# Optimization experiments

Hardware: AMD Instinct MI355X
Metric: run time of the kernel (lower is better)

## Reference

```python
import jax, jax.numpy as jnp
import numpy as np

DIM = 1024
H = 56
NS = 32            # n_state == head_v_dim
KEY_DIM = H * NS   # 1792
D_INNER = H * NS   # 1792
T_LEN = 2048
B = 4


def _xavier(key, fan_out, fan_in):
    bound = (6.0 / (fan_in + fan_out)) ** 0.5
    return jax.random.uniform(key, (fan_out, fan_in), jnp.float32, -bound, bound)


def setup_inputs() -> dict:
    key = jax.random.key(0)
    ks = jax.random.split(key, 8)
    x = jax.random.normal(ks[0], (T_LEN, B, DIM), jnp.float32)
    S = jnp.zeros((B, H, NS, NS), jnp.float32)
    Wq = _xavier(ks[1], KEY_DIM, DIM)
    Wk = _xavier(ks[2], KEY_DIM, DIM)
    Wv = _xavier(ks[3], D_INNER, DIM)
    Wa = _xavier(ks[4], H, DIM)
    Wout = _xavier(ks[5], DIM, D_INNER)
    A_log = jax.random.uniform(ks[6], (H,), jnp.float32, -5.0, -1.0)
    dt_bias = jax.random.uniform(ks[7], (H,), jnp.float32, 0.5, 1.5)
    return {"x": x, "S": S, "Wq": Wq, "Wk": Wk, "Wv": Wv, "Wa": Wa,
            "A_log": A_log, "dt_bias": dt_bias, "Wout": Wout}


def _l2norm(t):
    # matches F.normalize(dim=-1): x / max(||x||, 1e-12)
    n = jnp.sqrt(jnp.sum(t * t, axis=-1, keepdims=True))
    return t / jnp.maximum(n, 1e-12)


def reference(x, S, Wq, Wk, Wv, Wa, A_log, dt_bias, Wout):
    T, Bb, _ = x.shape
    q = jax.nn.silu(x @ Wq.T).reshape(T, Bb, H, NS)
    k = jax.nn.silu(x @ Wk.T).reshape(T, Bb, H, NS)
    v = jax.nn.silu(x @ Wv.T).reshape(T, Bb, H, NS)
    q = _l2norm(q)
    k = _l2norm(k)
    a = x @ Wa.T                                   # [T,B,H]
    dt = jax.nn.softplus(a + dt_bias)
    decay = jnp.exp(-jnp.exp(A_log) * dt)          # [T,B,H]

    def step(S_t, inp):
        k_t, v_t, q_t, d_t = inp                   # [B,H,NS], [B,H,NS], [B,H,NS], [B,H]
        retrieved = jnp.einsum('bhij,bhi->bhj', S_t, k_t)   # S^T k
        delta = v_t - retrieved
        outer = k_t[..., :, None] * delta[..., None, :]     # [B,H,NS,NS] = k ox delta
        S_t = S_t + jnp.tanh(d_t[..., None, None] * S_t + outer)
        Sq = jnp.einsum('bhij,bhi->bhj', S_t, q_t)
        return S_t, Sq

    S_new, out = jax.lax.scan(step, S, (k, v, q, decay))
    out = out.reshape(T, Bb, D_INNER) @ Wout.T     # [T,B,dim]
    return out, S_new
```

## Files before the change

kernel.cpp:

```cpp
#include <hip/hip_runtime.h>


typedef __attribute__((ext_vector_type(8))) __bf16 bf16x8;
typedef __attribute__((ext_vector_type(8))) _Float16 f16x8;
typedef __attribute__((ext_vector_type(4))) float f32x4;
typedef __attribute__((ext_vector_type(2))) float f32x2;

#define T_LEN 2048
#define BB 4
#define HH 56
#define NS 32
#define DIM 1024
#define KD 1792
#define MROWS 8192
#define CH 16
#define NCHUNK (T_LEN / CH)

#define VMCNT(N) asm volatile("s_waitcnt vmcnt(" #N ")" ::: "memory")
#define LGKM(N)  asm volatile("s_waitcnt lgkmcnt(" #N ")" ::: "memory")
#define SB       __builtin_amdgcn_sched_barrier(0)

__device__ __forceinline__ float bf2f(unsigned short u) {
    return __uint_as_float(((unsigned int)u) << 16);
}
__device__ __forceinline__ unsigned short f2bf(float f) {
    unsigned int u = __float_as_uint(f);
    u += 0x7fffu + ((u >> 16) & 1u);
    return (unsigned short)(u >> 16);
}
__device__ __forceinline__ unsigned short f2h(float f) {
    union { _Float16 h; unsigned short u; } cv;
    cv.h = (_Float16)f;
    return cv.u;
}
__device__ __forceinline__ float h2f(unsigned short u) {
    union { unsigned short u; _Float16 h; } cv;
    cv.u = u;
    return (float)cv.h;
}

__device__ __forceinline__ float tanh_fast(float x) {
    float e = __builtin_amdgcn_exp2f(x * 2.885390081777927f);
    float r = __builtin_amdgcn_rcpf(e + 1.0f);
    return fmaf(-2.0f, r, 1.0f);
}

__device__ __forceinline__ float dpp_sum16(float x) {
    int t;
    t = __builtin_amdgcn_update_dpp(0, __float_as_int(x), 0xB1, 0xf, 0xf, true);
    x += __int_as_float(t);
    t = __builtin_amdgcn_update_dpp(0, __float_as_int(x), 0x4E, 0xf, 0xf, true);
    x += __int_as_float(t);
    t = __builtin_amdgcn_update_dpp(0, __float_as_int(x), 0x141, 0xf, 0xf, true);
    x += __int_as_float(t);
    t = __builtin_amdgcn_update_dpp(0, __float_as_int(x), 0x140, 0xf, 0xf, true);
    x += __int_as_float(t);
    return x;
}

__device__ __forceinline__ void gload_lds16(const void* g, void* l) {
    __builtin_amdgcn_global_load_lds(
        (const __attribute__((address_space(1))) unsigned int*)g,
        (__attribute__((address_space(3))) unsigned int*)l, 16, 0, 0);
}
__device__ __forceinline__ void gload_lds4(const void* g, void* l) {
    __builtin_amdgcn_global_load_lds(
        (const __attribute__((address_space(1))) unsigned int*)g,
        (__attribute__((address_space(3))) unsigned int*)l, 4, 0, 0);
}

__device__ __forceinline__ unsigned lds_off(const void* p) {
    return (unsigned)(unsigned long long)
        (const __attribute__((address_space(3))) char*)p;
}

template <int OFF>
__device__ __forceinline__ f32x4 dsr128(unsigned a) {
    f32x4 r;
    asm volatile("ds_read_b128 %0, %1 offset:%2" : "=v"(r) : "v"(a), "n"(OFF));
    return r;
}
template <int OFF>
__device__ __forceinline__ f32x2 dsr64f(unsigned a) {
    f32x2 r;
    asm volatile("ds_read_b64 %0, %1 offset:%2" : "=v"(r) : "v"(a), "n"(OFF));
    return r;
}
template <int OFF>
__device__ __forceinline__ unsigned dsr32u(unsigned a) {
    unsigned r;
    asm volatile("ds_read_b32 %0, %1 offset:%2" : "=v"(r) : "v"(a), "n"(OFF));
    return r;
}
template <int OFF>
__device__ __forceinline__ float dsr32f(unsigned a) {
    float r;
    asm volatile("ds_read_b32 %0, %1 offset:%2" : "=v"(r) : "v"(a), "n"(OFF));
    return r;
}

__global__ void cast_split3_kernel(const float* __restrict__ in,
                                   unsigned short* __restrict__ hi,
                                   unsigned short* __restrict__ lo,
                                   unsigned short* __restrict__ h16, int n8) {
    int i = blockIdx.x * blockDim.x + threadIdx.x;
    if (i >= n8) return;
    const float4* p = (const float4*)in + (size_t)i * 2;
    float4 a = p[0], b = p[1];
    float xs[8] = {a.x, a.y, a.z, a.w, b.x, b.y, b.z, b.w};
    unsigned int ho[4], lv[4], hv[4];
#pragma unroll
    for (int c = 0; c < 4; ++c) {
        unsigned short h0 = f2bf(xs[2 * c]);
        unsigned short h1 = f2bf(xs[2 * c + 1]);
        unsigned short l0 = f2bf(xs[2 * c] - bf2f(h0));
        unsigned short l1 = f2bf(xs[2 * c + 1] - bf2f(h1));
        ho[c] = (unsigned int)h0 | ((unsigned int)h1 << 16);
        lv[c] = (unsigned int)l0 | ((unsigned int)l1 << 16);
        hv[c] = (unsigned int)f2h(xs[2 * c]) | ((unsigned int)f2h(xs[2 * c + 1]) << 16);
    }
    ((uint4*)hi)[i]  = (uint4){ho[0], ho[1], ho[2], ho[3]};
    ((uint4*)lo)[i]  = (uint4){lv[0], lv[1], lv[2], lv[3]};
    ((uint4*)h16)[i] = (uint4){hv[0], hv[1], hv[2], hv[3]};
}

__global__ void cast_split_kernel(const float* __restrict__ in,
                                  unsigned short* __restrict__ hi,
                                  unsigned short* __restrict__ lo, int n8) {
    int i = blockIdx.x * blockDim.x + threadIdx.x;
    if (i >= n8) return;
    const float4* p = (const float4*)in + (size_t)i * 2;
    float4 a = p[0], b = p[1];
    float xs[8] = {a.x, a.y, a.z, a.w, b.x, b.y, b.z, b.w};
    unsigned int ho[4], lv[4];
#pragma unroll
    for (int c = 0; c < 4; ++c) {
        unsigned short h0 = f2bf(xs[2 * c]);
        unsigned short h1 = f2bf(xs[2 * c + 1]);
        unsigned short l0 = f2bf(xs[2 * c] - bf2f(h0));
        unsigned short l1 = f2bf(xs[2 * c + 1] - bf2f(h1));
        ho[c] = (unsigned int)h0 | ((unsigned int)h1 << 16);
        lv[c] = (unsigned int)l0 | ((unsigned int)l1 << 16);
    }
    ((uint4*)hi)[i] = (uint4){ho[0], ho[1], ho[2], ho[3]};
    ((uint4*)lo)[i] = (uint4){lv[0], lv[1], lv[2], lv[3]};
}

__global__ void cast_half_kernel(const float* __restrict__ in,
                                 unsigned short* __restrict__ out, int n8) {
    int i = blockIdx.x * blockDim.x + threadIdx.x;
    if (i >= n8) return;
    const float4* p = (const float4*)in + (size_t)i * 2;
    float4 a = p[0], b = p[1];
    uint4 o;
    o.x = (unsigned int)f2h(a.x) | ((unsigned int)f2h(a.y) << 16);
    o.y = (unsigned int)f2h(a.z) | ((unsigned int)f2h(a.w) << 16);
    o.z = (unsigned int)f2h(b.x) | ((unsigned int)f2h(b.y) << 16);
    o.w = (unsigned int)f2h(b.z) | ((unsigned int)f2h(b.w) << 16);
    ((uint4*)out)[i] = o;
}

__device__ __forceinline__ void gemm_split(
    const unsigned short* __restrict__ Ah, const unsigned short* __restrict__ Al,
    const unsigned short* __restrict__ Bh, const unsigned short* __restrict__ Bl,
    int m0, int n0, int K, int bmax,
    unsigned short* AsH, unsigned short* AsL,
    unsigned short* BsH, unsigned short* BsL,
    f32x4 (&acc)[4][4]) {
    const int tid  = threadIdx.x;
    const int lane = tid & 63;
    const int wave = tid >> 6;
    const int wm = wave >> 1, wn = wave & 1;
    const int lr = lane & 15, lkb = lane >> 4;

#pragma unroll
    for (int fr = 0; fr < 4; ++fr)
#pragma unroll
        for (int fc = 0; fc < 4; ++fc) acc[fr][fc] = (f32x4){0.f, 0.f, 0.f, 0.f};

    auto stage = [&](int kt) {
#pragma unroll
        for (int c = 0; c < 2; ++c) {
            int i = c * 256 + tid;
            int r = i >> 2, kk = (i & 3) << 3;
            size_t ao = (size_t)(m0 + r) * K + kt + kk;
            int br = n0 + r; if (br > bmax) br = bmax;
            size_t bo = (size_t)br * K + kt + kk;
            gload_lds16(Ah + ao, AsH + i * 8);
            gload_lds16(Al + ao, AsL + i * 8);
            gload_lds16(Bh + bo, BsH + i * 8);
            gload_lds16(Bl + bo, BsL + i * 8);
        }
    };

    stage(0);
    const int nk = K >> 5;
    for (int t = 0; t < nk; ++t) {
        __syncthreads();
        bf16x8 ah[4], al[4], bh[4], bl[4];
#pragma unroll
        for (int f = 0; f < 4; ++f) {
            int ai = (wm * 64 + f * 16 + lr) * 32 + lkb * 8;
            int bi = (wn * 64 + f * 16 + lr) * 32 + lkb * 8;
            ah[f] = *(const bf16x8*)(AsH + ai);
            al[f] = *(const bf16x8*)(AsL + ai);
            bh[f] = *(const bf16x8*)(BsH + bi);
            bl[f] = *(const bf16x8*)(BsL + bi);
        }
#pragma unroll
        for (int fr = 0; fr < 4; ++fr)
#pragma unroll
            for (int fc = 0; fc < 4; ++fc) {
                acc[fr][fc] = __builtin_amdgcn_mfma_f32_16x16x32_bf16(
                    ah[fr], bh[fc], acc[fr][fc], 0, 0, 0);
                acc[fr][fc] = __builtin_amdgcn_mfma_f32_16x16x32_bf16(
                    ah[fr], bl[fc], acc[fr][fc], 0, 0, 0);
                acc[fr][fc] = __builtin_amdgcn_mfma_f32_16x16x32_bf16(
                    al[fr], bh[fc], acc[fr][fc], 0, 0, 0);
            }
        __syncthreads();
        if (t + 1 < nk) stage((t + 1) << 5);
    }
}

__global__ __launch_bounds__(256) void proj_split_kernel(
    const unsigned short* __restrict__ xh, const unsigned short* __restrict__ xl,
    const unsigned short* __restrict__ Wh, const unsigned short* __restrict__ Wl,
    const unsigned short* __restrict__ Wah, const unsigned short* __restrict__ Wal,
    const float* __restrict__ A_log, const float* __restrict__ dt_bias,
    float* __restrict__ dstF, float* __restrict__ decayb, int knorm) {
    __shared__ __align__(16) unsigned short AsH[128 * 32];
    __shared__ __align__(16) unsigned short AsL[128 * 32];
    __shared__ __align__(16) unsigned short BsH[128 * 32];
    __shared__ __align__(16) unsigned short BsL[128 * 32];

    const int tile = blockIdx.x;
    const bool isdecay = (tile == 14);
    int m0 = blockIdx.y * 128;
    int n0 = isdecay ? 0 : tile * 128;
    int bmax = isdecay ? (HH - 1) : (KD - 1);
    const unsigned short* Bh = isdecay ? Wah : Wh;
    const unsigned short* Bl = isdecay ? Wal : Wl;

    f32x4 acc[4][4];
    gemm_split(xh, xl, Bh, Bl, m0, n0, DIM, bmax, AsH, AsL, BsH, BsL, acc);

    const int lane = threadIdx.x & 63, wave = threadIdx.x >> 6;
    const int wm = wave >> 1, wn = wave & 1, lr = lane & 15, lkb = lane >> 4;

    if (isdecay) {
#pragma unroll
        for (int fr = 0; fr < 4; ++fr)
#pragma unroll
            for (int fc = 0; fc < 4; ++fc)
#pragma unroll
                for (int v = 0; v < 4; ++v) {
                    int m = m0 + wm * 64 + fr * 16 + lkb * 4 + v;
                    int n = n0 + wn * 64 + fc * 16 + lr;
                    int t = m >> 2, b = m & 3;
                    if (n < HH) {
                        float z = acc[fr][fc][v] + dt_bias[n];
                        float sp = (z > 20.f) ? z : log1pf(__expf(z));
                        decayb[((size_t)(b * HH + n)) * T_LEN + t] =
                            __expf(-__expf(A_log[n]) * sp);
                    }
                }
        return;
    }

    if (knorm) {
#pragma unroll
        for (int fr = 0; fr < 4; ++fr)
#pragma unroll
            for (int hc = 0; hc < 2; ++hc)
#pragma unroll
                for (int v = 0; v < 4; ++v) {
                    float yA = acc[fr][2 * hc][v];
                    float yB = acc[fr][2 * hc + 1][v];
                    float sA = yA / (1.f + __expf(-yA));
                    float sB = yB / (1.f + __expf(-yB));
                    float ss = fmaf(sA, sA, sB * sB);
                    ss = dpp_sum16(ss);
                    float sc = 1.f / fmaxf(sqrtf(ss), 1e-12f);
                    int m = m0 + wm * 64 + fr * 16 + lkb * 4 + v;
                    int t = m >> 2, b = m & 3;
                    int h = ((n0 + wn * 64) >> 5) + hc;
                    size_t ro = (((size_t)(b * HH + h)) * T_LEN + t) * NS;
                    dstF[ro + lr]      = sA * sc;
                    dstF[ro + lr + 16] = sB * sc;
                }
    } else {
#pragma unroll
        for (int fr = 0; fr < 4; ++fr)
#pragma unroll
            for (int fc = 0; fc < 4; ++fc)
#pragma unroll
                for (int v = 0; v < 4; ++v) {
                    int m = m0 + wm * 64 + fr * 16 + lkb * 4 + v;
                    int n = n0 + wn * 64 + fc * 16 + lr;
                    int t = m >> 2, b = m & 3;
                    int h = n >> 5, i = n & 31;
                    float y = acc[fr][fc][v];
                    float s = y / (1.f + __expf(-y));
                    dstF[(((size_t)(b * HH + h)) * T_LEN + t) * NS + i] = s;
                }
    }
}

__global__ __launch_bounds__(256) void q_gemm_f16_kernel(
    const unsigned short* __restrict__ xf, const unsigned short* __restrict__ Wqf,
    unsigned short* __restrict__ dstH) {
    __shared__ __align__(16) unsigned short As[128 * 32];
    __shared__ __align__(16) unsigned short Bs[128 * 32];
    int m0 = blockIdx.y * 128, n0 = blockIdx.x * 128;

    const int tid  = threadIdx.x;
    const int lane = tid & 63;
    const int wave = tid >> 6;
    const int wm = wave >> 1, wn = wave & 1;
    const int lr = lane & 15, lkb = lane >> 4;

    f32x4 acc[4][4];
#pragma unroll
    for (int fr = 0; fr < 4; ++fr)
#pragma unroll
        for (int fc = 0; fc < 4; ++fc) acc[fr][fc] = (f32x4){0.f, 0.f, 0.f, 0.f};

    auto stage = [&](int kt) {
#pragma unroll
        for (int c = 0; c < 2; ++c) {
            int i = c * 256 + tid;
            int r = i >> 2, kk = (i & 3) << 3;
            gload_lds16(xf + (size_t)(m0 + r) * DIM + kt + kk, As + i * 8);
            gload_lds16(Wqf + (size_t)(n0 + r) * DIM + kt + kk, Bs + i * 8);
        }
    };

    stage(0);
    const int nk = DIM >> 5;
    for (int t = 0; t < nk; ++t) {
        __syncthreads();
        f16x8 af[4], bf[4];
#pragma unroll
        for (int f = 0; f < 4; ++f) {
            af[f] = *(const f16x8*)(As + (wm * 64 + f * 16 + lr) * 32 + lkb * 8);
            bf[f] = *(const f16x8*)(Bs + (wn * 64 + f * 16 + lr) * 32 + lkb * 8);
        }
#pragma unroll
        for (int fr = 0; fr < 4; ++fr)
#pragma unroll
            for (int fc = 0; fc < 4; ++fc)
                acc[fr][fc] = __builtin_amdgcn_mfma_f32_16x16x32_f16(
                    af[fr], bf[fc], acc[fr][fc], 0, 0, 0);
        __syncthreads();
        if (t + 1 < nk) stage((t + 1) << 5);
    }

#pragma unroll
    for (int fr = 0; fr < 4; ++fr)
#pragma unroll
        for (int hc = 0; hc < 2; ++hc)
#pragma unroll
            for (int v = 0; v < 4; ++v) {
                float yA = acc[fr][2 * hc][v];
                float yB = acc[fr][2 * hc + 1][v];
                float sA = yA / (1.f + __expf(-yA));
                float sB = yB / (1.f + __expf(-yB));
                float ss = fmaf(sA, sA, sB * sB);
                ss = dpp_sum16(ss);
                float sc = 1.f / fmaxf(sqrtf(ss), 1e-12f);
                int m = m0 + wm * 64 + fr * 16 + lkb * 4 + v;
                int t = m >> 2, b = m & 3;
                int h = ((n0 + wn * 64) >> 5) + hc;
                size_t ro = (((size_t)(b * HH + h)) * T_LEN + t) * NS;
                dstH[ro + lr]      = f2h(sA * sc);
                dstH[ro + lr + 16] = f2h(sB * sc);
            }
}

__global__ __launch_bounds__(256) void out_gemm_kernel(
    const unsigned short* __restrict__ Sq, const unsigned short* __restrict__ Wo,
    float* __restrict__ out) {
    __shared__ __align__(16) unsigned short As[128 * 32];
    __shared__ __align__(16) unsigned short Bs[128 * 32];
    int m0 = blockIdx.y * 128, n0 = blockIdx.x * 128;

    const int tid  = threadIdx.x;
    const int lane = tid & 63;
    const int wave = tid >> 6;
    const int wm = wave >> 1, wn = wave & 1;
    const int lr = lane & 15, lkb = lane >> 4;

    f32x4 acc[4][4];
#pragma unroll
    for (int fr = 0; fr < 4; ++fr)
#pragma unroll
        for (int fc = 0; fc < 4; ++fc) acc[fr][fc] = (f32x4){0.f, 0.f, 0.f, 0.f};

    auto stage = [&](int kt) {
#pragma unroll
        for (int c = 0; c < 2; ++c) {
            int i = c * 256 + tid;
            int r = i >> 2, kk = (i & 3) << 3;
            gload_lds16(Sq + (size_t)(m0 + r) * KD + kt + kk, As + i * 8);
            gload_lds16(Wo + (size_t)(n0 + r) * KD + kt + kk, Bs + i * 8);
        }
    };

    stage(0);
    const int nk = KD >> 5;
    for (int t = 0; t < nk; ++t) {
        __syncthreads();
        f16x8 af[4], bf[4];
#pragma unroll
        for (int f = 0; f < 4; ++f) {
            af[f] = *(const f16x8*)(As + (wm * 64 + f * 16 + lr) * 32 + lkb * 8);
            bf[f] = *(const f16x8*)(Bs + (wn * 64 + f * 16 + lr) * 32 + lkb * 8);
        }
#pragma unroll
        for (int fr = 0; fr < 4; ++fr)
#pragma unroll
            for (int fc = 0; fc < 4; ++fc)
                acc[fr][fc] = __builtin_amdgcn_mfma_f32_16x16x32_f16(
                    af[fr], bf[fc], acc[fr][fc], 0, 0, 0);
        __syncthreads();
        if (t + 1 < nk) stage((t + 1) << 5);
    }

#pragma unroll
    for (int fr = 0; fr < 4; ++fr)
#pragma unroll
        for (int fc = 0; fc < 4; ++fc)
#pragma unroll
            for (int v = 0; v < 4; ++v) {
                int m = m0 + wm * 64 + fr * 16 + lkb * 4 + v;
                int n = n0 + wn * 64 + fc * 16 + lr;
                out[(size_t)m * DIM + n] = acc[fr][fc][v];
            }
}

__global__ __launch_bounds__(512, 1) void scan_kernel(
    const float* __restrict__ kf, const unsigned short* __restrict__ qh,
    const float* __restrict__ vf, const float* __restrict__ decayb,
    const float* __restrict__ S0, unsigned short* __restrict__ Sq,
    float* __restrict__ Sout) {
    __shared__ __align__(16) float          kbuf[4][CH][NS];
    __shared__ __align__(16) float          vbuf[4][CH][NS];
    __shared__ __align__(16) unsigned short qbuf[4][CH][NS];
    __shared__ __align__(16) float          dbuf[4][64];

    const int bh = blockIdx.x;
    const int b = bh / HH, h = bh - b * HH;
    const int tid = threadIdx.x;
    const int lane = tid & 63, wave = tid >> 6;
    const int col = tid >> 4;
    const int ii  = tid & 15;
    const int i0  = ii * 2;

    const float* Sp = S0 + (size_t)bh * NS * NS;
    float s0 = Sp[(i0 + 0) * NS + col];
    float s1 = Sp[(i0 + 1) * NS + col];

    const size_t base  = (size_t)bh * T_LEN * NS;
    const size_t dbase = (size_t)bh * T_LEN;
    const size_t cbcol = (size_t)h * NS;

    const unsigned kb0 = lds_off(&kbuf[0][0][0]) + (unsigned)ii * 8;
    const unsigned qb0 = lds_off(&qbuf[0][0][0]) + (unsigned)ii * 4;
    const unsigned vb0 = lds_off(&vbuf[0][0][0]) + (unsigned)col * 4;
    const unsigned db0 = lds_off(&dbuf[0][0]);

    auto stage = [&](int c) {
        int s = c & 3;
        if (wave == 0) {
            gload_lds16(kf + base + (size_t)c * 512 + lane * 4,
                        &kbuf[s][0][0] + lane * 4);
        } else if (wave == 1) {
            gload_lds16(kf + base + (size_t)c * 512 + 256 + lane * 4,
                        &kbuf[s][8][0] + lane * 4);
        } else if (wave == 2) {
            gload_lds16(vf + base + (size_t)c * 512 + lane * 4,
                        &vbuf[s][0][0] + lane * 4);
        } else if (wave == 3) {
            gload_lds16(vf + base + (size_t)c * 512 + 256 + lane * 4,
                        &vbuf[s][8][0] + lane * 4);
        } else if (wave == 4) {
            gload_lds16(qh + base + (size_t)c * 512 + lane * 8,
                        &qbuf[s][0][0] + lane * 8);
        } else if (wave == 5) {
            gload_lds4(decayb + dbase + (size_t)c * CH + lane,
                       &dbuf[s][0] + lane);
        }
    };

    stage(0);
    stage(1);
    VMCNT(0);
    __builtin_amdgcn_s_barrier();

    for (int c = 0; c < NCHUNK; ++c) {
        if (c + 2 < NCHUNK) stage(c + 2);
        if (wave < 6) { VMCNT(18); } else { VMCNT(16); }
        __builtin_amdgcn_s_barrier();
        SB;

        const int s = c & 3;
        const unsigned kb = kb0 + (unsigned)s * (CH * NS * 4);
        const unsigned qb = qb0 + (unsigned)s * (CH * NS * 2);
        const unsigned vb = vb0 + (unsigned)s * (CH * NS * 4);
        const unsigned db = db0 + (unsigned)s * 256;

        f32x2 kA[4], kB[4]; unsigned qA[4], qB[4]; float vA[4], vB[4];
        f32x4 dA, dB;

#define LDG(KK, QQ, VV, DV, g)                                          \
        KK[0] = dsr64f<((g) * 4 + 0) * 128>(kb);                        \
        KK[1] = dsr64f<((g) * 4 + 1) * 128>(kb);                        \
        KK[2] = dsr64f<((g) * 4 + 2) * 128>(kb);                        \
        KK[3] = dsr64f<((g) * 4 + 3) * 128>(kb);                        \
        QQ[0] = dsr32u<((g) * 4 + 0) * 64>(qb);                         \
        QQ[1] = dsr32u<((g) * 4 + 1) * 64>(qb);                         \
        QQ[2] = dsr32u<((g) * 4 + 2) * 64>(qb);                         \
        QQ[3] = dsr32u<((g) * 4 + 3) * 64>(qb);                         \
        VV[0] = dsr32f<((g) * 4 + 0) * 128>(vb);                        \
        VV[1] = dsr32f<((g) * 4 + 1) * 128>(vb);                        \
        VV[2] = dsr32f<((g) * 4 + 2) * 128>(vb);                        \
        VV[3] = dsr32f<((g) * 4 + 3) * 128>(vb);                        \
        DV    = dsr128<(g) * 16>(db);

#define CMP(KK, QQ, VV, DV, g)                                          \
        {                                                               \
            _Pragma("unroll")                                           \
            for (int p = 0; p < 4; ++p) {                               \
                const int t = c * CH + (g) * 4 + p;                     \
                float k0 = KK[p][0], k1 = KK[p][1];                     \
                float q0 = h2f((unsigned short)(QQ[p] & 0xffff));       \
                float q1 = h2f((unsigned short)(QQ[p] >> 16));          \
                float vj = VV[p];                                       \
                float d  = DV[p];                                       \
                float r = fmaf(k1, s1, k0 * s0);                        \
                r = dpp_sum16(r);                                       \
                float delta = vj - r;                                   \
                float a0 = fmaf(d, s0, k0 * delta);                     \
                float a1 = fmaf(d, s1, k1 * delta);                     \
                s0 += tanh_fast(a0); s1 += tanh_fast(a1);               \
                float o = fmaf(q1, s1, q0 * s0);                        \
                o = dpp_sum16(o);                                       \
                if (ii == 0) {                                          \
                    size_t ro = ((size_t)t * BB + b) * KD + cbcol;      \
                    Sq[ro + col] = f2h(o);                              \
                }                                                       \
            }                                                           \
        }

        LDG(kA, qA, vA, dA, 0);
        LDG(kB, qB, vB, dB, 1);
        LGKM(13); SB;
        CMP(kA, qA, vA, dA, 0);
        LDG(kA, qA, vA, dA, 2);
        LGKM(13); SB;
        CMP(kB, qB, vB, dB, 1);
        LDG(kB, qB, vB, dB, 3);
        LGKM(13); SB;
        CMP(kA, qA, vA, dA, 2);
        LGKM(0); SB;
        CMP(kB, qB, vB, dB, 3);
#undef LDG
#undef CMP
    }

    float* so = Sout + (size_t)bh * NS * NS;
    so[(i0 + 0) * NS + col] = s0;
    so[(i0 + 1) * NS + col] = s1;
}

extern "C" void kernel_launch(void* const* d_in, const int* in_sizes, int n_in,
                              void* d_out, int out_size, void* d_ws, size_t ws_size,
                              hipStream_t stream) {
    const float* x       = (const float*)d_in[0];
    const float* S0      = (const float*)d_in[1];
    const float* Wq      = (const float*)d_in[2];
    const float* Wk      = (const float*)d_in[3];
    const float* Wv      = (const float*)d_in[4];
    const float* Wa      = (const float*)d_in[5];
    const float* A_log   = (const float*)d_in[6];
    const float* dt_bias = (const float*)d_in[7];
    const float* Wout    = (const float*)d_in[8];

    float* out  = (float*)d_out;
    float* Sout = out + (size_t)T_LEN * BB * DIM;

    char* w = (char*)d_ws;
    auto alloc = [&](size_t bytes) {
        char* p = w; w += (bytes + 255) & ~(size_t)255; return p;
    };
    unsigned short* xh  = (unsigned short*)alloc((size_t)MROWS * DIM * 2);
    unsigned short* xl  = (unsigned short*)alloc((size_t)MROWS * DIM * 2);
    unsigned short* Wbh = (unsigned short*)alloc((size_t)KD * DIM * 2);
    unsigned short* Wbl = (unsigned short*)alloc((size_t)KD * DIM * 2);
    unsigned short* Wah = (unsigned short*)alloc((size_t)HH * DIM * 2);
    unsigned short* Wal = (unsigned short*)alloc((size_t)HH * DIM * 2);
    float* kf           = (float*)alloc((size_t)MROWS * KD * 4);
    float* vf           = (float*)alloc((size_t)MROWS * KD * 4);
    unsigned short* Woh = (unsigned short*)alloc((size_t)DIM * KD * 2);
    unsigned short* Sq   = xh;
    unsigned short* xf16 = (unsigned short*)vf;

    unsigned short* qh  = (unsigned short*)d_out;
    float* decayb       = (float*)((char*)d_out + (size_t)MROWS * KD * 2);

    {
        int n8 = (int)((size_t)MROWS * DIM / 8);
        cast_split3_kernel<<<(n8 + 255) / 256, 256, 0, stream>>>(x, xh, xl, xf16, n8);
    }
    {
        int n8 = (int)((size_t)KD * DIM / 8);
        cast_half_kernel<<<(n8 + 255) / 256, 256, 0, stream>>>(Wq, Wbh, n8);
        q_gemm_f16_kernel<<<dim3(14, 64), 256, 0, stream>>>(xf16, Wbh, qh);
    }
    {
        int n8 = (int)((size_t)KD * DIM / 8);
        cast_split_kernel<<<(n8 + 255) / 256, 256, 0, stream>>>(Wk, Wbh, Wbl, n8);
        int n8a = (int)((size_t)HH * DIM / 8);
        cast_split_kernel<<<(n8a + 255) / 256, 256, 0, stream>>>(Wa, Wah, Wal, n8a);
        proj_split_kernel<<<dim3(15, 64), 256, 0, stream>>>(
            xh, xl, Wbh, Wbl, Wah, Wal, A_log, dt_bias, kf, decayb, 1);
    }
    {
        int n8 = (int)((size_t)KD * DIM / 8);
        cast_split_kernel<<<(n8 + 255) / 256, 256, 0, stream>>>(Wv, Wbh, Wbl, n8);
        proj_split_kernel<<<dim3(14, 64), 256, 0, stream>>>(
            xh, xl, Wbh, Wbl, Wah, Wal, A_log, dt_bias, vf, decayb, 0);
    }
    {
        int n8 = (int)((size_t)DIM * KD / 8);
        cast_half_kernel<<<(n8 + 255) / 256, 256, 0, stream>>>(Wout, Woh, n8);
    }
    scan_kernel<<<BB * HH, 512, 0, stream>>>(kf, qh, vf, decayb, S0, Sq, Sout);
    out_gemm_kernel<<<dim3(8, 64), 256, 0, stream>>>(Sq, Woh, out);
}
```

Baseline: 739.7 us.

## Map one state element per thread in scan with 1024-thread blocks

The scan kernel goes from 512 threads, each holding two state elements, to 1024 threads, each holding one. The 32-row reduction now uses a 16-lane DPP sum followed by a permlane32 swap, and the k and q loads from LDS shrink to 32-bit and 16-bit reads. This halves the serial per-thread work on each timestep's critical path. In exchange it adds a cross-half permlane step to each reduction and doubles the number of waves contending for one CU's issue slots, since there are 224 blocks with one per CU.

```diff
diff --git a/kernel.cpp b/kernel.cpp
--- a/kernel.cpp
+++ b/kernel.cpp
@@ -5,6 +5,7 @@
 typedef __attribute__((ext_vector_type(8))) _Float16 f16x8;
 typedef __attribute__((ext_vector_type(4))) float f32x4;
 typedef __attribute__((ext_vector_type(2))) float f32x2;
+typedef __attribute__((ext_vector_type(2))) unsigned int u32x2v;
 
 #define T_LEN 2048
 #define BB 4
@@ -58,6 +59,12 @@
     return x;
 }
 
+__device__ __forceinline__ float swap_sum32(float x) {
+    u32x2v pr = __builtin_amdgcn_permlane32_swap(
+        __float_as_uint(x), __float_as_uint(x), false, false);
+    return __uint_as_float(pr[0]) + __uint_as_float(pr[1]);
+}
+
 __device__ __forceinline__ void gload_lds16(const void* g, void* l) {
     __builtin_amdgcn_global_load_lds(
         (const __attribute__((address_space(1))) unsigned int*)g,
@@ -81,15 +88,9 @@
     return r;
 }
 template <int OFF>
-__device__ __forceinline__ f32x2 dsr64f(unsigned a) {
-    f32x2 r;
-    asm volatile("ds_read_b64 %0, %1 offset:%2" : "=v"(r) : "v"(a), "n"(OFF));
-    return r;
-}
-template <int OFF>
-__device__ __forceinline__ unsigned dsr32u(unsigned a) {
+__device__ __forceinline__ unsigned dsr16(unsigned a) {
     unsigned r;
-    asm volatile("ds_read_b32 %0, %1 offset:%2" : "=v"(r) : "v"(a), "n"(OFF));
+    asm volatile("ds_read_u16 %0, %1 offset:%2" : "=v"(r) : "v"(a), "n"(OFF));
     return r;
 }
 template <int OFF>
@@ -439,7 +440,7 @@
             }
 }
 
-__global__ __launch_bounds__(512, 1) void scan_kernel(
+__global__ __launch_bounds__(1024, 1) void scan_kernel(
     const float* __restrict__ kf, const unsigned short* __restrict__ qh,
     const float* __restrict__ vf, const float* __restrict__ decayb,
     const float* __restrict__ S0, unsigned short* __restrict__ Sq,
@@ -453,20 +454,18 @@
     const int b = bh / HH, h = bh - b * HH;
     const int tid = threadIdx.x;
     const int lane = tid & 63, wave = tid >> 6;
-    const int col = tid >> 4;
-    const int ii  = tid & 15;
-    const int i0  = ii * 2;
+    const int col = (wave << 1) | ((lane >> 4) & 1);
+    const int e   = (lane & 15) | ((lane >> 5) << 4);
 
     const float* Sp = S0 + (size_t)bh * NS * NS;
-    float s0 = Sp[(i0 + 0) * NS + col];
-    float s1 = Sp[(i0 + 1) * NS + col];
+    float s0 = Sp[(size_t)e * NS + col];
 
     const size_t base  = (size_t)bh * T_LEN * NS;
     const size_t dbase = (size_t)bh * T_LEN;
     const size_t cbcol = (size_t)h * NS;
 
-    const unsigned kb0 = lds_off(&kbuf[0][0][0]) + (unsigned)ii * 8;
-    const unsigned qb0 = lds_off(&qbuf[0][0][0]) + (unsigned)ii * 4;
+    const unsigned kb0 = lds_off(&kbuf[0][0][0]) + (unsigned)e * 4;
+    const unsigned qb0 = lds_off(&qbuf[0][0][0]) + (unsigned)e * 2;
     const unsigned vb0 = lds_off(&vbuf[0][0][0]) + (unsigned)col * 4;
     const unsigned db0 = lds_off(&dbuf[0][0]);
 
@@ -500,7 +499,7 @@
 
     for (int c = 0; c < NCHUNK; ++c) {
         if (c + 2 < NCHUNK) stage(c + 2);
-        if (wave < 6) { VMCNT(18); } else { VMCNT(16); }
+        if (wave < 6) { VMCNT(18); }
         __builtin_amdgcn_s_barrier();
         SB;
 
@@ -510,18 +509,18 @@
         const unsigned vb = vb0 + (unsigned)s * (CH * NS * 4);
         const unsigned db = db0 + (unsigned)s * 256;
 
-        f32x2 kA[4], kB[4]; unsigned qA[4], qB[4]; float vA[4], vB[4];
+        float kA[4], kB[4]; unsigned qA[4], qB[4]; float vA[4], vB[4];
         f32x4 dA, dB;
 
 #define LDG(KK, QQ, VV, DV, g)                                          \
-        KK[0] = dsr64f<((g) * 4 + 0) * 128>(kb);                        \
-        KK[1] = dsr64f<((g) * 4 + 1) * 128>(kb);                        \
-        KK[2] = dsr64f<((g) * 4 + 2) * 128>(kb);                        \
-        KK[3] = dsr64f<((g) * 4 + 3) * 128>(kb);                        \
-        QQ[0] = dsr32u<((g) * 4 + 0) * 64>(qb);                         \
-        QQ[1] = dsr32u<((g) * 4 + 1) * 64>(qb);                         \
-        QQ[2] = dsr32u<((g) * 4 + 2) * 64>(qb);                         \
-        QQ[3] = dsr32u<((g) * 4 + 3) * 64>(qb);                         \
+        KK[0] = dsr32f<((g) * 4 + 0) * 128>(kb);                        \
+        KK[1] = dsr32f<((g) * 4 + 1) * 128>(kb);                        \
+        KK[2] = dsr32f<((g) * 4 + 2) * 128>(kb);                        \
+        KK[3] = dsr32f<((g) * 4 + 3) * 128>(kb);                        \
+        QQ[0] = dsr16<((g) * 4 + 0) * 64>(qb);                          \
+        QQ[1] = dsr16<((g) * 4 + 1) * 64>(qb);                          \
+        QQ[2] = dsr16<((g) * 4 + 2) * 64>(qb);                          \
+        QQ[3] = dsr16<((g) * 4 + 3) * 64>(qb);                          \
         VV[0] = dsr32f<((g) * 4 + 0) * 128>(vb);                        \
         VV[1] = dsr32f<((g) * 4 + 1) * 128>(vb);                        \
         VV[2] = dsr32f<((g) * 4 + 2) * 128>(vb);                        \
@@ -533,20 +532,16 @@
             _Pragma("unroll")                                           \
             for (int p = 0; p < 4; ++p) {                               \
                 const int t = c * CH + (g) * 4 + p;                     \
-                float k0 = KK[p][0], k1 = KK[p][1];                     \
-                float q0 = h2f((unsigned short)(QQ[p] & 0xffff));       \
-                float q1 = h2f((unsigned short)(QQ[p] >> 16));          \
+                float k0 = KK[p];                                       \
+                float q0 = h2f((unsigned short)QQ[p]);                  \
                 float vj = VV[p];                                       \
                 float d  = DV[p];                                       \
-                float r = fmaf(k1, s1, k0 * s0);                        \
-                r = dpp_sum16(r);                                       \
+                float r = swap_sum32(dpp_sum16(k0 * s0));               \
                 float delta = vj - r;                                   \
                 float a0 = fmaf(d, s0, k0 * delta);                     \
-                float a1 = fmaf(d, s1, k1 * delta);                     \
-                s0 += tanh_fast(a0); s1 += tanh_fast(a1);               \
-                float o = fmaf(q1, s1, q0 * s0);                        \
-                o = dpp_sum16(o);                                       \
-                if (ii == 0) {                                          \
+                s0 += tanh_fast(a0);                                    \
+                float o = swap_sum32(dpp_sum16(q0 * s0));               \
+                if (e == 0) {                                           \
                     size_t ro = ((size_t)t * BB + b) * KD + cbcol;      \
                     Sq[ro + col] = f2h(o);                              \
                 }                                                       \
@@ -570,8 +565,7 @@
     }
 
     float* so = Sout + (size_t)bh * NS * NS;
-    so[(i0 + 0) * NS + col] = s0;
-    so[(i0 + 1) * NS + col] = s1;
+    so[(size_t)e * NS + col] = s0;
 }
 
 extern "C" void kernel_launch(void* const* d_in, const int* in_sizes, int n_in,
@@ -636,6 +630,6 @@
         int n8 = (int)((size_t)DIM * KD / 8);
         cast_half_kernel<<<(n8 + 255) / 256, 256, 0, stream>>>(Wout, Woh, n8);
     }
-    scan_kernel<<<BB * HH, 512, 0, stream>>>(kf, qh, vf, decayb, S0, Sq, Sout);
+    scan_kernel<<<BB * HH, 1024, 0, stream>>>(kf, qh, vf, decayb, S0, Sq, Sout);
     out_gemm_kernel<<<dim3(8, 64), 256, 0, stream>>>(Sq, Woh, out);
 }
```

New measurement: 934.8 us. 26.4% more time.
